# Performance work log

Hardware: AMD Instinct MI355X
Metric: run time of the kernel (lower is better)

## Reference

```python
import jax, jax.numpy as jnp
import numpy as np

B, T, F, H = 16, 512, 32, 128
EPS = 1e-5


def _layer_norm(y, g, b):
    mu = jnp.mean(y, axis=-1, keepdims=True)
    var = jnp.mean(jnp.square(y - mu), axis=-1, keepdims=True)
    return (y - mu) * jax.lax.rsqrt(var + EPS) * g + b


def setup_inputs() -> dict:
    key = jax.random.key(0)
    ks = jax.random.split(key, 16)
    s = 0.1  # small param scale
    return {
        "x": jax.random.normal(ks[0], (B, T, F), jnp.float32),
        # weight GRN (input_size == hidden == F, skip is Identity)
        "wg_fc1_w": jax.random.normal(ks[1], (F, F), jnp.float32) * s,
        "wg_fc1_b": jnp.zeros((F,), jnp.float32),
        "wg_fc2_w": jax.random.normal(ks[2], (2 * F, F), jnp.float32) * s,
        "wg_fc2_b": jnp.zeros((2 * F,), jnp.float32),
        "wg_ln_g": jnp.ones((F,), jnp.float32),
        "wg_ln_b": jnp.zeros((F,), jnp.float32),
        # per-feature GRNs (input_size=1 -> hidden H), batched over F
        "f_fc1_w": jax.random.normal(ks[3], (F, H), jnp.float32) * s,   # torch Linear(1,H).weight squeezed
        "f_fc1_b": jax.random.normal(ks[4], (F, H), jnp.float32) * s,
        "f_fc2_w": jax.random.normal(ks[5], (F, 2 * H, H), jnp.float32) * s,
        "f_fc2_b": jax.random.normal(ks[6], (F, 2 * H), jnp.float32) * s,
        "f_skip_w": jax.random.normal(ks[7], (F, H), jnp.float32) * s,  # Linear(1,H).weight squeezed
        "f_skip_b": jax.random.normal(ks[8], (F, H), jnp.float32) * s,
        "f_ln_g": jnp.ones((F, H), jnp.float32),
        "f_ln_b": jnp.zeros((F, H), jnp.float32),
    }


def reference(x, wg_fc1_w, wg_fc1_b, wg_fc2_w, wg_fc2_b, wg_ln_g, wg_ln_b,
              f_fc1_w, f_fc1_b, f_fc2_w, f_fc2_b, f_skip_w, f_skip_b,
              f_ln_g, f_ln_b):
    # --- weight GRN over the feature axis: [B,T,F] -> [B,T,F] ---
    h = jax.nn.elu(jnp.einsum('btf,gf->btg', x, wg_fc1_w) + wg_fc1_b)
    h2 = jnp.einsum('btg,kg->btk', h, wg_fc2_w) + wg_fc2_b  # [B,T,2F]
    a, g = jnp.split(h2, 2, axis=-1)
    glu = a * jax.nn.sigmoid(g)
    weights = jax.nn.softmax(_layer_norm(x + glu, wg_ln_g, wg_ln_b), axis=-1)  # [B,T,F]

    # --- all F per-feature GRNs batched (input width 1) ---
    xe = x[..., None]                                   # [B,T,F,1]
    h = jax.nn.elu(xe * f_fc1_w + f_fc1_b)              # [B,T,F,H]
    h2 = jnp.einsum('btfh,fgh->btfg', h, f_fc2_w) + f_fc2_b  # [B,T,F,2H]
    a, g = jnp.split(h2, 2, axis=-1)
    glu = a * jax.nn.sigmoid(g)                         # [B,T,F,H]
    res = xe * f_skip_w + f_skip_b                      # [B,T,F,H]
    y = _layer_norm(res + glu, f_ln_g, f_ln_b)          # per-feature LN params [F,H]

    # --- softmax-weighted combine ---
    return jnp.einsum('btf,btfh->bth', weights, y)      # [B,T,H]
```

## Files before the change

kernel.cpp:

```cpp
#include <hip/hip_runtime.h>
#include <cstdint>
#include <cstddef>

#define EPS 1e-5f

typedef float    f4     __attribute__((ext_vector_type(4)));
typedef float    f2     __attribute__((ext_vector_type(2)));
typedef _Float16 half8  __attribute__((ext_vector_type(8)));
typedef _Float16 half4  __attribute__((ext_vector_type(4)));

#define S_XS 33
#define F_BLK 8
#define CHUNK 8192

#define GLD_LDS16(gp, lp)                                        \
    __builtin_amdgcn_global_load_lds(                            \
        (const __attribute__((address_space(1))) void*)(gp),     \
        (__attribute__((address_space(3))) void*)(lp), 16, 0, 0)

__global__ __launch_bounds__(256) void k_conv(const float* __restrict__ in,
                                              _Float16* __restrict__ out) {
    int t = blockIdx.x * 256 + threadIdx.x;
    int j0 = (t & 3) * 8;
    int g  = (t >> 2) & 255;
    int fk = t >> 10;
    int f = fk >> 2, kq = fk & 3;
    const float* ip = in + ((size_t)f * 256 + g) * 128 + kq * 32 + j0;
    f4 v0 = *(const f4*)ip, v1 = *(const f4*)(ip + 4);
    half8 h;
    #pragma unroll
    for (int i = 0; i < 4; ++i) { h[i] = (_Float16)v0[i]; h[4 + i] = (_Float16)v1[i]; }
    *(half8*)(out + (size_t)t * 8) = h;
}

__global__ __launch_bounds__(256) void k_weights(
    const float* __restrict__ x, const float* __restrict__ w1,
    const float* __restrict__ b1, const float* __restrict__ w2,
    const float* __restrict__ b2, const float* __restrict__ lng,
    const float* __restrict__ lnb, float* __restrict__ wts) {
    __shared__ float w1s[32 * S_XS];
    __shared__ float w2s[64 * S_XS];
    __shared__ float xsW[32 * S_XS];

    const int tid = threadIdx.x;
    const int lane = tid & 63;
    const int f = lane & 31;
    const int wv = tid >> 6;
    const int row0 = blockIdx.x * 32;

    for (int i = tid; i < 1024; i += 256) {
        int r = i >> 5, c = i & 31;
        w1s[r * S_XS + c] = w1[i];
        xsW[r * S_XS + c] = x[(size_t)row0 * 32 + i];
    }
    for (int i = tid; i < 2048; i += 256) {
        int r = i >> 5, c = i & 31;
        w2s[r * S_XS + c] = w2[i];
    }
    const float b1f = b1[f], b2a = b2[f], b2g = b2[f + 32];
    const float lgf = lng[f], lbf = lnb[f];
    __syncthreads();

    for (int rr = 0; rr < 8; ++rr) {
        const int r = wv * 8 + rr;
        float acc = b1f;
        #pragma unroll
        for (int k = 0; k < 32; ++k)
            acc = fmaf(w1s[f * S_XS + k], xsW[r * S_XS + k], acc);
        float hval = acc > 0.f ? acc : __expf(acc) - 1.f;

        float a = b2a, g = b2g;
        #pragma unroll
        for (int k = 0; k < 32; ++k) {
            float hk = __shfl(hval, k, 64);
            a = fmaf(w2s[f * S_XS + k], hk, a);
            g = fmaf(w2s[(f + 32) * S_XS + k], hk, g);
        }
        float xv = xsW[r * S_XS + f];
        float v = xv + a * (1.f / (1.f + __expf(-g)));

        float s = v;
        #pragma unroll
        for (int o = 1; o < 64; o <<= 1) s += __shfl_xor(s, o, 64);
        float mu = s * (1.f / 64.f);
        float d = v - mu;
        float sq = d * d;
        #pragma unroll
        for (int o = 1; o < 64; o <<= 1) sq += __shfl_xor(sq, o, 64);
        float y = d * rsqrtf(sq * (1.f / 64.f) + EPS) * lgf + lbf;

        float m = y;
        #pragma unroll
        for (int o = 1; o < 64; o <<= 1) m = fmaxf(m, __shfl_xor(m, o, 64));
        float e = __expf(y - m);
        float se = e;
        #pragma unroll
        for (int o = 1; o < 64; o <<= 1) se += __shfl_xor(se, o, 64);
        if (lane < 32) wts[(size_t)(row0 + r) * 32 + f] = e * 2.f / se;
    }
}

__global__ __launch_bounds__(256, 3) void k_main(
    const float* __restrict__ x,
    const _Float16* __restrict__ w2c,
    const float* __restrict__ fc1w,
    const float* __restrict__ fc1b,
    const float* __restrict__ fc2b,
    const float* __restrict__ skw,
    const float* __restrict__ skb,
    const float* __restrict__ lng,
    const float* __restrict__ lnb,
    const float* __restrict__ wts,
    float* __restrict__ out)
{
    __shared__ __align__(16) _Float16 bchunk[2][CHUNK];
    __shared__ float xs[64 * S_XS];
    __shared__ float wss[64 * S_XS];

    const int tid = threadIdx.x;
    const int tile = blockIdx.x >> 2;
    const int fbase = (blockIdx.x & 3) * F_BLK;
    const int row0 = tile * 64;

    for (int i = tid; i < 2048; i += 256) {
        int r = i >> 5, c = i & 31;
        xs[r * S_XS + c] = x[(size_t)row0 * 32 + i];
        wss[r * S_XS + c] = wts[(size_t)row0 * 32 + i];
    }

    const int lane = tid & 63;
    const int wv = tid >> 6;
    const int l15 = lane & 15;
    const int q = lane >> 4;
    const int rA = wv * 16 + l15;

    const _Float16* w2base = w2c + (size_t)fbase * 4 * CHUNK;

    auto stage = [&](int cg, int b) {
        const _Float16* gp = w2base + (size_t)cg * CHUNK;
        #pragma unroll
        for (int r = 0; r < 4; ++r) {
            const _Float16* g = gp + (r * 256 + tid) * 8;
            _Float16* l = &bchunk[b][(r * 256 + tid) * 8];
            GLD_LDS16(g, l);
        }
    };

    float out_acc[8][4];
    #pragma unroll
    for (int nt = 0; nt < 8; ++nt)
        #pragma unroll
        for (int rg = 0; rg < 4; ++rg) out_acc[nt][rg] = 0.f;

    stage(0, 0);
    __syncthreads();

    int cg = 0;
    for (int fi = 0; fi < F_BLK; ++fi) {
        const int f = fbase + fi;
        const float xvA = xs[rA * S_XS + f];

        f4 acc[16];
        {
            f4 z; z[0] = 0.f; z[1] = 0.f; z[2] = 0.f; z[3] = 0.f;
            #pragma unroll
            for (int nt = 0; nt < 16; ++nt) acc[nt] = z;
        }

        #pragma unroll
        for (int kq = 0; kq < 4; ++kq, ++cg) {
            if (cg + 1 < F_BLK * 4) stage(cg + 1, (cg + 1) & 1);

            half8 A;
            {
                const float* wp = fc1w + f * 128 + kq * 32 + 8 * q;
                const float* bp = fc1b + f * 128 + kq * 32 + 8 * q;
                f4 w0 = *(const f4*)wp, w1v = *(const f4*)(wp + 4);
                f4 b0 = *(const f4*)bp, b1v = *(const f4*)(bp + 4);
                #pragma unroll
                for (int j = 0; j < 4; ++j) {
                    float t0 = fmaf(xvA, w0[j], b0[j]);
                    float t1 = fmaf(xvA, w1v[j], b1v[j]);
                    t0 = t0 > 0.f ? t0 : __expf(t0) - 1.f;
                    t1 = t1 > 0.f ? t1 : __expf(t1) - 1.f;
                    A[j] = (_Float16)t0;
                    A[4 + j] = (_Float16)t1;
                }
            }

            const _Float16* bb = &bchunk[cg & 1][8 * q + l15 * 32];
            half8 B[8];
            #pragma unroll
            for (int nt = 0; nt < 8; ++nt)
                B[nt] = *(const half8*)(bb + nt * (16 * 32));
            #pragma unroll
            for (int nt = 0; nt < 8; ++nt)
                acc[nt] = __builtin_amdgcn_mfma_f32_16x16x32_f16(A, B[nt], acc[nt], 0, 0, 0);
            #pragma unroll
            for (int nt = 0; nt < 8; ++nt)
                B[nt] = *(const half8*)(bb + (nt + 8) * (16 * 32));
            #pragma unroll
            for (int nt = 0; nt < 8; ++nt)
                acc[nt + 8] = __builtin_amdgcn_mfma_f32_16x16x32_f16(A, B[nt], acc[nt + 8], 0, 0, 0);

            __syncthreads();
        }

        float xr[4], wrow[4];
        #pragma unroll
        for (int rg = 0; rg < 4; ++rg) {
            xr[rg] = xs[(wv * 16 + 4 * q + rg) * S_XS + f];
            wrow[rg] = wss[(wv * 16 + 4 * q + rg) * S_XS + f];
        }
        float vv[8][4];
        float s[4] = {0.f, 0.f, 0.f, 0.f}, sq[4] = {0.f, 0.f, 0.f, 0.f};
        #pragma unroll
        for (int nt = 0; nt < 8; ++nt) {
            const int h = nt * 16 + l15;
            float ba = fc2b[f * 256 + h];
            float bg = fc2b[f * 256 + 128 + h];
            float sw = skw[f * 128 + h];
            float sb = skb[f * 128 + h];
            #pragma unroll
            for (int rg = 0; rg < 4; ++rg) {
                float a = acc[nt][rg] + ba;
                float g = acc[nt + 8][rg] + bg;
                float sig = 1.f / (1.f + __expf(-g));
                float val = fmaf(xr[rg], sw, sb) + a * sig;
                vv[nt][rg] = val;
                s[rg] += val;
                sq[rg] = fmaf(val, val, sq[rg]);
            }
        }
        #pragma unroll
        for (int o = 1; o < 16; o <<= 1) {
            #pragma unroll
            for (int rg = 0; rg < 4; ++rg) {
                s[rg] += __shfl_xor(s[rg], o, 64);
                sq[rg] += __shfl_xor(sq[rg], o, 64);
            }
        }
        float mu[4], wr[4];
        #pragma unroll
        for (int rg = 0; rg < 4; ++rg) {
            mu[rg] = s[rg] * (1.f / 128.f);
            float var = sq[rg] * (1.f / 128.f) - mu[rg] * mu[rg];
            wr[rg] = wrow[rg] * rsqrtf(fmaxf(var, 0.f) + EPS);
        }
        #pragma unroll
        for (int nt = 0; nt < 8; ++nt) {
            const int h = nt * 16 + l15;
            float lg = lng[f * 128 + h];
            float lb = lnb[f * 128 + h];
            #pragma unroll
            for (int rg = 0; rg < 4; ++rg) {
                float u = (vv[nt][rg] - mu[rg]) * wr[rg];
                out_acc[nt][rg] = fmaf(u, lg, fmaf(wrow[rg], lb, out_acc[nt][rg]));
            }
        }
    }

    #pragma unroll
    for (int nt = 0; nt < 8; ++nt) {
        #pragma unroll
        for (int rg = 0; rg < 4; ++rg) {
            const int r = row0 + wv * 16 + 4 * q + rg;
            atomicAdd(&out[(size_t)r * 128 + nt * 16 + l15], out_acc[nt][rg]);
        }
    }
}

extern "C" void kernel_launch(void* const* d_in, const int* in_sizes, int n_in,
                              void* d_out, int out_size, void* d_ws, size_t ws_size,
                              hipStream_t stream) {
    const float* x     = (const float*)d_in[0];
    const float* wg1w  = (const float*)d_in[1];
    const float* wg1b  = (const float*)d_in[2];
    const float* wg2w  = (const float*)d_in[3];
    const float* wg2b  = (const float*)d_in[4];
    const float* wglng = (const float*)d_in[5];
    const float* wglnb = (const float*)d_in[6];
    const float* fc1w  = (const float*)d_in[7];
    const float* fc1b  = (const float*)d_in[8];
    const float* fc2w  = (const float*)d_in[9];
    const float* fc2b  = (const float*)d_in[10];
    const float* skw   = (const float*)d_in[11];
    const float* skb   = (const float*)d_in[12];
    const float* lng   = (const float*)d_in[13];
    const float* lnb   = (const float*)d_in[14];
    float* out = (float*)d_out;

    _Float16* w2c = (_Float16*)d_ws;
    float* wts = (float*)((char*)d_ws + (2u << 20));

    k_conv<<<dim3(512), dim3(256), 0, stream>>>(fc2w, w2c);
    k_weights<<<dim3(256), dim3(256), 0, stream>>>(x, wg1w, wg1b, wg2w, wg2b,
                                                   wglng, wglnb, wts);
    hipMemsetAsync(out, 0, (size_t)out_size * sizeof(float), stream);
    k_main<<<dim3(512), dim3(256), 0, stream>>>(x, w2c, fc1w, fc1b, fc2b,
                                                skw, skb, lng, lnb, wts, out);
}
```

Measured before the change: 178.2 us.

## Make fc2 weights LDS-resident per feature, replace atomics with fp16 partials

The main kernel is reorganised so that each block handles a single feature. That feature's full fc2 weight matrix (64KB fp16) is loaded into LDS once, and the block sweeps 512 rows with no per-chunk barriers. Bias, skip and layer-norm parameters are hoisted into registers, and x and the softmax weights are read from feature-major transposed copies written by a merged prep kernel that also does the fp16 weight conversion. When the workspace is large enough, per-feature outputs are written as fp16 partials and summed by a separate reduce kernel instead of float atomics. This trades the atomic traffic for roughly 64MB each of partial writes and reads, and accepts some fp16 rounding in the partial sums.

Result: slower. 423.9 us (+137.9%).

```diff
diff --git a/kernel.cpp b/kernel.cpp
--- a/kernel.cpp
+++ b/kernel.cpp
@@ -4,49 +4,52 @@
 
 #define EPS 1e-5f
 
-typedef float    f4     __attribute__((ext_vector_type(4)));
-typedef float    f2     __attribute__((ext_vector_type(2)));
-typedef _Float16 half8  __attribute__((ext_vector_type(8)));
-typedef _Float16 half4  __attribute__((ext_vector_type(4)));
+typedef float    f4    __attribute__((ext_vector_type(4)));
+typedef _Float16 half8 __attribute__((ext_vector_type(8)));
+typedef _Float16 half4 __attribute__((ext_vector_type(4)));
 
 #define S_XS 33
-#define F_BLK 8
-#define CHUNK 8192
 
 #define GLD_LDS16(gp, lp)                                        \
     __builtin_amdgcn_global_load_lds(                            \
         (const __attribute__((address_space(1))) void*)(gp),     \
         (__attribute__((address_space(3))) void*)(lp), 16, 0, 0)
 
-__global__ __launch_bounds__(256) void k_conv(const float* __restrict__ in,
-                                              _Float16* __restrict__ out) {
-    int t = blockIdx.x * 256 + threadIdx.x;
-    int j0 = (t & 3) * 8;
-    int g  = (t >> 2) & 255;
-    int fk = t >> 10;
-    int f = fk >> 2, kq = fk & 3;
-    const float* ip = in + ((size_t)f * 256 + g) * 128 + kq * 32 + j0;
-    f4 v0 = *(const f4*)ip, v1 = *(const f4*)(ip + 4);
-    half8 h;
-    #pragma unroll
-    for (int i = 0; i < 4; ++i) { h[i] = (_Float16)v0[i]; h[4 + i] = (_Float16)v1[i]; }
-    *(half8*)(out + (size_t)t * 8) = h;
-}
-
-__global__ __launch_bounds__(256) void k_weights(
+__global__ __launch_bounds__(256) void k_prep(
+    const float* __restrict__ in_w2, _Float16* __restrict__ w2c,
     const float* __restrict__ x, const float* __restrict__ w1,
     const float* __restrict__ b1, const float* __restrict__ w2,
     const float* __restrict__ b2, const float* __restrict__ lng,
-    const float* __restrict__ lnb, float* __restrict__ wts) {
+    const float* __restrict__ lnb,
+    float* __restrict__ x_t, float* __restrict__ wts_t)
+{
     __shared__ float w1s[32 * S_XS];
     __shared__ float w2s[64 * S_XS];
     __shared__ float xsW[32 * S_XS];
-
+    __shared__ float ytile[32 * S_XS];
+
+    const int bid = blockIdx.x;
     const int tid = threadIdx.x;
+
+    if (bid < 512) {
+        int t = bid * 256 + tid;
+        int j0 = (t & 3) * 8;
+        int g  = (t >> 2) & 255;
+        int fk = t >> 10;
+        int f = fk >> 2, kq = fk & 3;
+        const float* ip = in_w2 + ((size_t)f * 256 + g) * 128 + kq * 32 + j0;
+        f4 v0 = *(const f4*)ip, v1 = *(const f4*)(ip + 4);
+        half8 h;
+        #pragma unroll
+        for (int i = 0; i < 4; ++i) { h[i] = (_Float16)v0[i]; h[4 + i] = (_Float16)v1[i]; }
+        *(half8*)(w2c + (size_t)t * 8) = h;
+        return;
+    }
+
     const int lane = tid & 63;
     const int f = lane & 31;
     const int wv = tid >> 6;
-    const int row0 = blockIdx.x * 32;
+    const int row0 = (bid - 512) * 32;
 
     for (int i = tid; i < 1024; i += 256) {
         int r = i >> 5, c = i & 31;
@@ -96,138 +99,113 @@
         float se = e;
         #pragma unroll
         for (int o = 1; o < 64; o <<= 1) se += __shfl_xor(se, o, 64);
-        if (lane < 32) wts[(size_t)(row0 + r) * 32 + f] = e * 2.f / se;
+        if (lane < 32) ytile[r * S_XS + f] = e * 2.f / se;
+    }
+    __syncthreads();
+    for (int i = tid; i < 1024; i += 256) {
+        int ff = i >> 5, r = i & 31;
+        x_t[(size_t)ff * 8192 + row0 + r]   = xsW[r * S_XS + ff];
+        wts_t[(size_t)ff * 8192 + row0 + r] = ytile[r * S_XS + ff];
     }
 }
 
-__global__ __launch_bounds__(256, 3) void k_main(
-    const float* __restrict__ x,
+__global__ __launch_bounds__(256, 2) void k_main(
     const _Float16* __restrict__ w2c,
-    const float* __restrict__ fc1w,
-    const float* __restrict__ fc1b,
+    const float* __restrict__ x_t,
+    const float* __restrict__ wts_t,
+    const float* __restrict__ fc1w, const float* __restrict__ fc1b,
     const float* __restrict__ fc2b,
-    const float* __restrict__ skw,
-    const float* __restrict__ skb,
-    const float* __restrict__ lng,
-    const float* __restrict__ lnb,
-    const float* __restrict__ wts,
-    float* __restrict__ out)
+    const float* __restrict__ skw, const float* __restrict__ skb,
+    const float* __restrict__ lng, const float* __restrict__ lnb,
+    _Float16* __restrict__ part,
+    float* __restrict__ out, int use_part)
 {
-    __shared__ __align__(16) _Float16 bchunk[2][CHUNK];
-    __shared__ float xs[64 * S_XS];
-    __shared__ float wss[64 * S_XS];
+    __shared__ __align__(16) _Float16 w2s[4 * 8192];
 
     const int tid = threadIdx.x;
-    const int tile = blockIdx.x >> 2;
-    const int fbase = (blockIdx.x & 3) * F_BLK;
-    const int row0 = tile * 64;
-
-    for (int i = tid; i < 2048; i += 256) {
-        int r = i >> 5, c = i & 31;
-        xs[r * S_XS + c] = x[(size_t)row0 * 32 + i];
-        wss[r * S_XS + c] = wts[(size_t)row0 * 32 + i];
-    }
+    const int f = blockIdx.x >> 4;
+    const int row0 = (blockIdx.x & 15) << 9;
+
+    const _Float16* wsrc = w2c + (size_t)f * 32768;
+    #pragma unroll
+    for (int i = 0; i < 16; ++i)
+        GLD_LDS16(wsrc + (i * 256 + tid) * 8, &w2s[(i * 256 + tid) * 8]);
 
     const int lane = tid & 63;
     const int wv = tid >> 6;
     const int l15 = lane & 15;
     const int q = lane >> 4;
-    const int rA = wv * 16 + l15;
-
-    const _Float16* w2base = w2c + (size_t)fbase * 4 * CHUNK;
-
-    auto stage = [&](int cg, int b) {
-        const _Float16* gp = w2base + (size_t)cg * CHUNK;
-        #pragma unroll
-        for (int r = 0; r < 4; ++r) {
-            const _Float16* g = gp + (r * 256 + tid) * 8;
-            _Float16* l = &bchunk[b][(r * 256 + tid) * 8];
-            GLD_LDS16(g, l);
-        }
-    };
-
-    float out_acc[8][4];
-    #pragma unroll
-    for (int nt = 0; nt < 8; ++nt)
-        #pragma unroll
-        for (int rg = 0; rg < 4; ++rg) out_acc[nt][rg] = 0.f;
-
-    stage(0, 0);
+
+    f4 w1r[4][2], b1r[4][2];
+    #pragma unroll
+    for (int kq = 0; kq < 4; ++kq) {
+        const float* wp = fc1w + f * 128 + kq * 32 + 8 * q;
+        const float* bp = fc1b + f * 128 + kq * 32 + 8 * q;
+        w1r[kq][0] = *(const f4*)wp;  w1r[kq][1] = *(const f4*)(wp + 4);
+        b1r[kq][0] = *(const f4*)bp;  b1r[kq][1] = *(const f4*)(bp + 4);
+    }
+    float ba[8], bg[8], swv[8], sbv[8], lgv[8], lbv[8];
+    #pragma unroll
+    for (int nt = 0; nt < 8; ++nt) {
+        const int h = nt * 16 + l15;
+        ba[nt]  = fc2b[f * 256 + h];
+        bg[nt]  = fc2b[f * 256 + 128 + h];
+        swv[nt] = skw[f * 128 + h];
+        sbv[nt] = skb[f * 128 + h];
+        lgv[nt] = lng[f * 128 + h];
+        lbv[nt] = lnb[f * 128 + h];
+    }
+    const float* xcol = x_t + (size_t)f * 8192 + row0;
+    const float* wcol = wts_t + (size_t)f * 8192 + row0;
+    const int boff = l15 * 32 + q * 8;
+
     __syncthreads();
 
-    int cg = 0;
-    for (int fi = 0; fi < F_BLK; ++fi) {
-        const int f = fbase + fi;
-        const float xvA = xs[rA * S_XS + f];
-
-        f4 acc[16];
-        {
-            f4 z; z[0] = 0.f; z[1] = 0.f; z[2] = 0.f; z[3] = 0.f;
-            #pragma unroll
-            for (int nt = 0; nt < 16; ++nt) acc[nt] = z;
-        }
-
-        #pragma unroll
-        for (int kq = 0; kq < 4; ++kq, ++cg) {
-            if (cg + 1 < F_BLK * 4) stage(cg + 1, (cg + 1) & 1);
-
-            half8 A;
-            {
-                const float* wp = fc1w + f * 128 + kq * 32 + 8 * q;
-                const float* bp = fc1b + f * 128 + kq * 32 + 8 * q;
-                f4 w0 = *(const f4*)wp, w1v = *(const f4*)(wp + 4);
-                f4 b0 = *(const f4*)bp, b1v = *(const f4*)(bp + 4);
+    for (int it = 0; it < 8; ++it) {
+        const int rb = wv * 128 + it * 16;
+
+        const float xvA = xcol[rb + l15];
+        half8 A[4];
+        #pragma unroll
+        for (int kq = 0; kq < 4; ++kq) {
+            #pragma unroll
+            for (int jj = 0; jj < 2; ++jj) {
                 #pragma unroll
                 for (int j = 0; j < 4; ++j) {
-                    float t0 = fmaf(xvA, w0[j], b0[j]);
-                    float t1 = fmaf(xvA, w1v[j], b1v[j]);
-                    t0 = t0 > 0.f ? t0 : __expf(t0) - 1.f;
-                    t1 = t1 > 0.f ? t1 : __expf(t1) - 1.f;
-                    A[j] = (_Float16)t0;
-                    A[4 + j] = (_Float16)t1;
+                    float t = fmaf(xvA, w1r[kq][jj][j], b1r[kq][jj][j]);
+                    t = t > 0.f ? t : __expf(t) - 1.f;
+                    A[kq][jj * 4 + j] = (_Float16)t;
                 }
             }
-
-            const _Float16* bb = &bchunk[cg & 1][8 * q + l15 * 32];
-            half8 B[8];
-            #pragma unroll
-            for (int nt = 0; nt < 8; ++nt)
-                B[nt] = *(const half8*)(bb + nt * (16 * 32));
-            #pragma unroll
-            for (int nt = 0; nt < 8; ++nt)
-                acc[nt] = __builtin_amdgcn_mfma_f32_16x16x32_f16(A, B[nt], acc[nt], 0, 0, 0);
-            #pragma unroll
-            for (int nt = 0; nt < 8; ++nt)
-                B[nt] = *(const half8*)(bb + (nt + 8) * (16 * 32));
-            #pragma unroll
-            for (int nt = 0; nt < 8; ++nt)
-                acc[nt + 8] = __builtin_amdgcn_mfma_f32_16x16x32_f16(A, B[nt], acc[nt + 8], 0, 0, 0);
-
-            __syncthreads();
-        }
-
-        float xr[4], wrow[4];
-        #pragma unroll
-        for (int rg = 0; rg < 4; ++rg) {
-            xr[rg] = xs[(wv * 16 + 4 * q + rg) * S_XS + f];
-            wrow[rg] = wss[(wv * 16 + 4 * q + rg) * S_XS + f];
-        }
-        float vv[8][4];
+        }
+
+        f4 acc[16];
+        #pragma unroll
+        for (int nt = 0; nt < 8; ++nt) {
+            #pragma unroll
+            for (int rg = 0; rg < 4; ++rg) { acc[nt][rg] = ba[nt]; acc[nt + 8][rg] = bg[nt]; }
+        }
+        #pragma unroll
+        for (int kq = 0; kq < 4; ++kq) {
+            #pragma unroll
+            for (int nt = 0; nt < 16; ++nt) {
+                half8 B = *(const half8*)&w2s[kq * 8192 + nt * 512 + boff];
+                acc[nt] = __builtin_amdgcn_mfma_f32_16x16x32_f16(A[kq], B, acc[nt], 0, 0, 0);
+            }
+        }
+
+        f4 xr = *(const f4*)(xcol + rb + 4 * q);
+        f4 wr = *(const f4*)(wcol + rb + 4 * q);
         float s[4] = {0.f, 0.f, 0.f, 0.f}, sq[4] = {0.f, 0.f, 0.f, 0.f};
         #pragma unroll
         for (int nt = 0; nt < 8; ++nt) {
-            const int h = nt * 16 + l15;
-            float ba = fc2b[f * 256 + h];
-            float bg = fc2b[f * 256 + 128 + h];
-            float sw = skw[f * 128 + h];
-            float sb = skb[f * 128 + h];
             #pragma unroll
             for (int rg = 0; rg < 4; ++rg) {
-                float a = acc[nt][rg] + ba;
-                float g = acc[nt + 8][rg] + bg;
+                float a = acc[nt][rg];
+                float g = acc[nt + 8][rg];
                 float sig = 1.f / (1.f + __expf(-g));
-                float val = fmaf(xr[rg], sw, sb) + a * sig;
-                vv[nt][rg] = val;
+                float val = fmaf(xr[rg], swv[nt], sbv[nt]) + a * sig;
+                acc[nt][rg] = val;
                 s[rg] += val;
                 sq[rg] = fmaf(val, val, sq[rg]);
             }
@@ -240,33 +218,73 @@
                 sq[rg] += __shfl_xor(sq[rg], o, 64);
             }
         }
-        float mu[4], wr[4];
+        float mu[4], c1[4];
         #pragma unroll
         for (int rg = 0; rg < 4; ++rg) {
             mu[rg] = s[rg] * (1.f / 128.f);
             float var = sq[rg] * (1.f / 128.f) - mu[rg] * mu[rg];
-            wr[rg] = wrow[rg] * rsqrtf(fmaxf(var, 0.f) + EPS);
-        }
-        #pragma unroll
-        for (int nt = 0; nt < 8; ++nt) {
-            const int h = nt * 16 + l15;
-            float lg = lng[f * 128 + h];
-            float lb = lnb[f * 128 + h];
-            #pragma unroll
-            for (int rg = 0; rg < 4; ++rg) {
-                float u = (vv[nt][rg] - mu[rg]) * wr[rg];
-                out_acc[nt][rg] = fmaf(u, lg, fmaf(wrow[rg], lb, out_acc[nt][rg]));
-            }
-        }
-    }
-
-    #pragma unroll
-    for (int nt = 0; nt < 8; ++nt) {
-        #pragma unroll
-        for (int rg = 0; rg < 4; ++rg) {
-            const int r = row0 + wv * 16 + 4 * q + rg;
-            atomicAdd(&out[(size_t)r * 128 + nt * 16 + l15], out_acc[nt][rg]);
-        }
+            c1[rg] = wr[rg] * rsqrtf(fmaxf(var, 0.f) + EPS);
+        }
+
+        if (use_part) {
+            #pragma unroll
+            for (int nt = 0; nt < 8; ++nt) {
+                half4 pk;
+                #pragma unroll
+                for (int rg = 0; rg < 4; ++rg) {
+                    float y = fmaf((acc[nt][rg] - mu[rg]) * c1[rg], lgv[nt],
+                                   wr[rg] * lbv[nt]);
+                    pk[rg] = (_Float16)y;
+                }
+                *(half4*)(part + ((size_t)f << 20) + ((size_t)(nt * 16 + l15) << 13)
+                          + row0 + rb + 4 * q) = pk;
+            }
+        } else {
+            #pragma unroll
+            for (int nt = 0; nt < 8; ++nt) {
+                #pragma unroll
+                for (int rg = 0; rg < 4; ++rg) {
+                    float y = fmaf((acc[nt][rg] - mu[rg]) * c1[rg], lgv[nt],
+                                   wr[rg] * lbv[nt]);
+                    atomicAdd(&out[(size_t)(row0 + rb + 4 * q + rg) * 128
+                                   + nt * 16 + l15], y);
+                }
+            }
+        }
+    }
+}
+
+__global__ __launch_bounds__(256) void k_reduce(const _Float16* __restrict__ part,
+                                                float* __restrict__ out) {
+    __shared__ float t[32 * 130];
+    const int tid = threadIdx.x;
+    const int row0 = blockIdx.x * 32;
+    #pragma unroll
+    for (int si = 0; si < 4; ++si) {
+        const int s = tid + 256 * si;
+        const int rowq = s & 7;
+        const int h = s >> 3;
+        f4 acc; acc[0] = 0.f; acc[1] = 0.f; acc[2] = 0.f; acc[3] = 0.f;
+        const _Float16* p = part + ((size_t)h << 13) + row0 + (rowq << 2);
+        #pragma unroll
+        for (int fq = 0; fq < 32; ++fq) {
+            half4 v = *(const half4*)(p + ((size_t)fq << 20));
+            acc[0] += (float)v[0]; acc[1] += (float)v[1];
+            acc[2] += (float)v[2]; acc[3] += (float)v[3];
+        }
+        #pragma unroll
+        for (int i = 0; i < 4; ++i)
+            t[(rowq * 4 + i) * 130 + h] = acc[i];
+    }
+    __syncthreads();
+    #pragma unroll
+    for (int p2 = 0; p2 < 4; ++p2) {
+        const int row = p2 * 8 + (tid >> 5);
+        const int h4 = (tid & 31) * 4;
+        f4 o;
+        #pragma unroll
+        for (int i = 0; i < 4; ++i) o[i] = t[row * 130 + h4 + i];
+        *(f4*)(out + (size_t)(row0 + row) * 128 + h4) = o;
     }
 }
 
@@ -290,13 +308,23 @@
     const float* lnb   = (const float*)d_in[14];
     float* out = (float*)d_out;
 
-    _Float16* w2c = (_Float16*)d_ws;
-    float* wts = (float*)((char*)d_ws + (2u << 20));
-
-    k_conv<<<dim3(512), dim3(256), 0, stream>>>(fc2w, w2c);
-    k_weights<<<dim3(256), dim3(256), 0, stream>>>(x, wg1w, wg1b, wg2w, wg2b,
-                                                   wglng, wglnb, wts);
-    hipMemsetAsync(out, 0, (size_t)out_size * sizeof(float), stream);
-    k_main<<<dim3(512), dim3(256), 0, stream>>>(x, w2c, fc1w, fc1b, fc2b,
-                                                skw, skb, lng, lnb, wts, out);
+    char* ws = (char*)d_ws;
+    _Float16* w2c  = (_Float16*)ws;
+    float* x_t     = (float*)(ws + (2u << 20));
+    float* wts_t   = (float*)(ws + (3u << 20));
+    _Float16* part = (_Float16*)(ws + (4u << 20));
+
+    const size_t need = (size_t)(4u << 20) + (size_t)32 * 8192 * 128 * 2;
+    const int fast = ws_size >= need;
+
+    k_prep<<<dim3(768), dim3(256), 0, stream>>>(fc2w, w2c, x, wg1w, wg1b,
+                                                wg2w, wg2b, wglng, wglnb,
+                                                x_t, wts_t);
+    if (!fast)
+        hipMemsetAsync(out, 0, (size_t)out_size * sizeof(float), stream);
+    k_main<<<dim3(512), dim3(256), 0, stream>>>(w2c, x_t, wts_t, fc1w, fc1b,
+                                                fc2b, skw, skb, lng, lnb,
+                                                part, out, fast);
+    if (fast)
+        k_reduce<<<dim3(256), dim3(256), 0, stream>>>(part, out);
 }
```
